# Performance work log

Measured on AMD Instinct MI355X. Metric: run time of the kernel, lower is better.

Reference implementation:

```python
import jax, jax.numpy as jnp
import numpy as np
from functools import partial

FACTOR = 5
N_HEADS = 16


def setup_inputs() -> dict:
    key = jax.random.key(0)
    ks = jax.random.split(key, 8)
    B, L, D = 4, 4096, 1024
    scale = 0.02
    return {
        "q": jax.random.normal(ks[0], (B, L, D), jnp.float32),
        "k": jax.random.normal(ks[1], (B, L, D), jnp.float32),
        "v": jax.random.normal(ks[2], (B, L, D), jnp.float32),
        "Wq": jax.random.normal(ks[3], (D, D), jnp.float32) * scale,
        "bq": jnp.zeros((D,), jnp.float32),
        "Wk": jax.random.normal(ks[4], (D, D), jnp.float32) * scale,
        "bk": jnp.zeros((D,), jnp.float32),
        "Wv": jax.random.normal(ks[5], (D, D), jnp.float32) * scale,
        "bv": jnp.zeros((D,), jnp.float32),
        "Wo": jax.random.normal(ks[6], (D, D), jnp.float32) * scale,
        "bo": jnp.zeros((D,), jnp.float32),
    }


def _time_delay_agg(values, corr):
    # values, corr: (B, H, L, C).  Faithful to the repo: the double mean
    # over dim=1 reduces head then LENGTH, leaving (B, C); top-k indices
    # therefore live in [0, C) and are reused as time delays.
    B, H, L, C = values.shape
    top_k = int(FACTOR * np.log(L + 1)) if L > 1 else 1
    top_k = max(1, min(top_k, L))
    mean_value = corr.mean(axis=1).mean(axis=1)          # (B, C)
    mean_across_batch = mean_value.mean(axis=0)          # (C,)
    actual_k = min(top_k, C)
    _, indices = jax.lax.top_k(mean_across_batch, actual_k)  # (k,)
    selected = mean_value[:, indices]                    # (B, k)
    weights = jax.nn.softmax(selected, axis=-1)          # (B, k)
    t = jnp.arange(L)

    def body(acc, inp):
        d, w = inp                                       # scalar delay, (B,) weight
        idx = (t + d) % L                                # circular shift == roll of doubled tensor
        acc = acc + values[:, :, idx, :] * w[:, None, None, None]
        return acc, None

    agg, _ = jax.lax.scan(body, jnp.zeros_like(values), (indices, weights.T))
    return agg


def reference(q, k, v, Wq, bq, Wk, bk, Wv, bv, Wo, bo):
    B, L, D = q.shape
    H = N_HEADS
    dk = D // H

    def proj(x, W, b):
        y = x @ W.T + b
        return y.reshape(B, L, H, dk).transpose(0, 2, 1, 3)  # (B,H,L,dk)

    Q = proj(q, Wq, bq).astype(jnp.float32)
    K = proj(k, Wk, bk).astype(jnp.float32)
    V = proj(v, Wv, bv).astype(jnp.float32)

    Qf = jnp.fft.rfft(Q, axis=2)
    Kf = jnp.fft.rfft(K, axis=2)
    R = jnp.fft.irfft(Qf * jnp.conj(Kf), n=L, axis=2)    # (B,H,L,dk) autocorrelation

    V_agg = _time_delay_agg(V, R)                        # (B,H,L,dk)
    V_agg = V_agg.transpose(0, 2, 1, 3).reshape(B, L, D)
    return V_agg @ Wo.T + bo
```

## Files before the change

kernel.cpp:

```cpp
#include <hip/hip_runtime.h>
#include <hip/hip_bf16.h>

#define Bn 4
#define Ln 4096
#define Dn 1024
#define Hn 16
#define KSEL 41
#define NT8 16

typedef __attribute__((ext_vector_type(8))) _Float16 f16x8;
typedef __attribute__((ext_vector_type(4))) float f32x4;

__device__ __forceinline__ unsigned short f2h(float f) {
    union { _Float16 h; unsigned short u; } c;
    c.h = (_Float16)f;
    return c.u;
}

__device__ __forceinline__ void gl2lds16(const unsigned short* g, unsigned short* l) {
    __builtin_amdgcn_global_load_lds(
        (const __attribute__((address_space(1))) unsigned int*)(uintptr_t)g,
        (__attribute__((address_space(3))) unsigned int*)(uintptr_t)l,
        16, 0, 0);
}
__device__ __forceinline__ void gl2lds16f(const float* g, float* l) {
    __builtin_amdgcn_global_load_lds(
        (const __attribute__((address_space(1))) unsigned int*)(uintptr_t)g,
        (__attribute__((address_space(3))) unsigned int*)(uintptr_t)l,
        16, 0, 0);
}

__global__ __launch_bounds__(256) void prework(const float* __restrict__ q,
                                               const float* __restrict__ k,
                                               const float* __restrict__ Wq_unused,
                                               const float* __restrict__ Wo,
                                               const float* __restrict__ Wv,
                                               const float* __restrict__ bv,
                                               const float* __restrict__ bo,
                                               float* __restrict__ part,
                                               unsigned short* __restrict__ Wcf,
                                               float* __restrict__ bc) {
    __shared__ __align__(16) unsigned short sAB[2][64 * 32];
    int bid = blockIdx.x;
    int tid = threadIdx.x;

    if (bid < 512) {
        int cx = bid & 63, tb = bid >> 6;
        int tensor = tb >> 2, b = tb & 3;
        const f32x4* src = (const f32x4*)((tensor ? k : q) + (size_t)b * Ln * Dn) + tid;
        int t0 = cx * 64;
        f32x4 a0 = (f32x4){0.f, 0.f, 0.f, 0.f};
        f32x4 a1 = (f32x4){0.f, 0.f, 0.f, 0.f};
        #pragma unroll 1
        for (int g = 0; g < 8; ++g) {
            const f32x4* p = src + (size_t)(t0 + g * 8) * 256;
            f32x4 v0 = __builtin_nontemporal_load(p + 0 * 256);
            f32x4 v1 = __builtin_nontemporal_load(p + 1 * 256);
            f32x4 v2 = __builtin_nontemporal_load(p + 2 * 256);
            f32x4 v3 = __builtin_nontemporal_load(p + 3 * 256);
            f32x4 v4 = __builtin_nontemporal_load(p + 4 * 256);
            f32x4 v5 = __builtin_nontemporal_load(p + 5 * 256);
            f32x4 v6 = __builtin_nontemporal_load(p + 6 * 256);
            f32x4 v7 = __builtin_nontemporal_load(p + 7 * 256);
            a0 += v0 + v2 + v4 + v6;
            a1 += v1 + v3 + v5 + v7;
        }
        f32x4 o = a0 + a1;
        ((f32x4*)part)[((size_t)tb * 64 + cx) * 256 + tid] = o;
    } else if (bid < 768) {
        unsigned short* sA = sAB[0];
        unsigned short* sB = sAB[1];
        int b2 = bid - 512;
        int n0 = (b2 >> 4) * 64, k0 = (b2 & 15) * 64;
        const int wv = tid >> 6, lane = tid & 63;
        const int wr = wv >> 1, wc = wv & 1;
        const int lrow = lane & 15, lk = (lane >> 4) * 8;
        const int ar0 = tid >> 3,  ac0 = (tid & 7) * 4;
        const int ar1 = (tid + 256) >> 3, ac1 = ((tid + 256) & 7) * 4;
        const int jr0 = tid >> 4,  kc0 = (tid & 15) * 4;
        const int jr1 = (tid + 256) >> 4, kc1 = ((tid + 256) & 15) * 4;
        f32x4 acc[2][2];
        #pragma unroll
        for (int i = 0; i < 2; ++i)
            #pragma unroll
            for (int j = 0; j < 2; ++j) acc[i][j] = (f32x4){0.f, 0.f, 0.f, 0.f};

        float4 avA, avB, bvA, bvB;
        auto LOADW = [&](int j0) {
            avA = *(const float4*)&Wo[(size_t)(n0 + ar0) * 1024 + j0 + ac0];
            avB = *(const float4*)&Wo[(size_t)(n0 + ar1) * 1024 + j0 + ac1];
            bvA = *(const float4*)&Wv[(size_t)(j0 + jr0) * 1024 + k0 + kc0];
            bvB = *(const float4*)&Wv[(size_t)(j0 + jr1) * 1024 + k0 + kc1];
        };
        LOADW(0);
        #pragma unroll 1
        for (int it = 0; it < 32; ++it) {
            ushort4 h;
            h.x = f2h(avA.x); h.y = f2h(avA.y); h.z = f2h(avA.z); h.w = f2h(avA.w);
            *(ushort4*)&sA[ar0 * 32 + ac0] = h;
            h.x = f2h(avB.x); h.y = f2h(avB.y); h.z = f2h(avB.z); h.w = f2h(avB.w);
            *(ushort4*)&sA[ar1 * 32 + ac1] = h;
            sB[(kc0 + 0) * 32 + jr0] = f2h(bvA.x);
            sB[(kc0 + 1) * 32 + jr0] = f2h(bvA.y);
            sB[(kc0 + 2) * 32 + jr0] = f2h(bvA.z);
            sB[(kc0 + 3) * 32 + jr0] = f2h(bvA.w);
            sB[(kc1 + 0) * 32 + jr1] = f2h(bvB.x);
            sB[(kc1 + 1) * 32 + jr1] = f2h(bvB.y);
            sB[(kc1 + 2) * 32 + jr1] = f2h(bvB.z);
            sB[(kc1 + 3) * 32 + jr1] = f2h(bvB.w);
            __syncthreads();
            if (it + 1 < 32) LOADW((it + 1) * 32);
            f16x8 af[2], bf[2];
            #pragma unroll
            for (int i = 0; i < 2; ++i)
                af[i] = *(const f16x8*)&sA[(wr * 32 + i * 16 + lrow) * 32 + lk];
            #pragma unroll
            for (int j = 0; j < 2; ++j)
                bf[j] = *(const f16x8*)&sB[(wc * 32 + j * 16 + lrow) * 32 + lk];
            #pragma unroll
            for (int i = 0; i < 2; ++i)
                #pragma unroll
                for (int j = 0; j < 2; ++j)
                    acc[i][j] = __builtin_amdgcn_mfma_f32_16x16x32_f16(af[i], bf[j], acc[i][j], 0, 0, 0);
            __syncthreads();
        }
        #pragma unroll
        for (int i = 0; i < 2; ++i) {
            int r0 = n0 + wr * 32 + i * 16 + (lane >> 4) * 4;
            #pragma unroll
            for (int j = 0; j < 2; ++j) {
                int c = k0 + wc * 32 + j * 16 + (lane & 15);
                #pragma unroll
                for (int r = 0; r < 4; ++r)
                    Wcf[(size_t)(r0 + r) * 1024 + c] = f2h(acc[i][j][r]);
            }
        }
    } else {
        float* s_bv = (float*)sAB;
        int b3 = bid - 768;
        for (int i = tid; i < 1024; i += 256) s_bv[i] = bv[i];
        __syncthreads();
        int wv2 = tid >> 6, lane = tid & 63;
        for (int rr = 0; rr < 4; ++rr) {
            int n = b3 * 16 + rr * 4 + wv2;
            float p = 0.f;
            for (int c = 0; c < 4; ++c) {
                float4 w4 = *(const float4*)(Wo + (size_t)n * 1024 + c * 256 + lane * 4);
                float4 s4 = *(const float4*)(s_bv + c * 256 + lane * 4);
                p += w4.x * s4.x + w4.y * s4.y + w4.z * s4.z + w4.w * s4.w;
            }
            for (int off = 1; off < 64; off <<= 1) p += __shfl_xor(p, off);
            if (lane == 0) bc[n] = p + bo[n];
        }
    }
}

__global__ void colsum_fin(const float* __restrict__ part, float* __restrict__ sums) {
    int tb = blockIdx.y; int d = blockIdx.x * 256 + threadIdx.x;
    float s = 0.f;
    for (int i = 0; i < 64; ++i) s += part[((size_t)tb * 64 + i) * 1024 + d];
    sums[(size_t)tb * 1024 + d] = s;
}

__global__ void proj_sums(const float* __restrict__ sums,
                          const float* __restrict__ Wq, const float* __restrict__ bq,
                          const float* __restrict__ Wk, const float* __restrict__ bk,
                          float* __restrict__ SQK) {
    int t = blockIdx.y;
    const float* W    = t ? Wk : Wq;
    const float* bias = t ? bk : bq;
    const float* sv   = sums + (size_t)t * 4 * 1024;
    __shared__ float s_sv[4 * 1024];
    for (int i = threadIdx.x; i < 4 * 1024; i += 256) s_sv[i] = sv[i];
    __syncthreads();
    int wave = threadIdx.x >> 6, lane = threadIdx.x & 63;
    for (int rr = 0; rr < 4; ++rr) {
        int j = blockIdx.x * 16 + rr * 4 + wave;
        float p[4] = {0.f, 0.f, 0.f, 0.f};
        for (int c = 0; c < 4; ++c) {
            float4 wv = *(const float4*)(W + (size_t)j * 1024 + c * 256 + lane * 4);
            #pragma unroll
            for (int b = 0; b < 4; ++b) {
                float4 s = *(const float4*)(s_sv + b * 1024 + c * 256 + lane * 4);
                p[b] += wv.x * s.x + wv.y * s.y + wv.z * s.z + wv.w * s.w;
            }
        }
        #pragma unroll
        for (int b = 0; b < 4; ++b)
            for (int off = 1; off < 64; off <<= 1) p[b] += __shfl_xor(p[b], off);
        if (lane == 0) {
            float bb = bias[j] * (float)Ln;
            #pragma unroll
            for (int b = 0; b < 4; ++b) SQK[((size_t)t * 4 + b) * 1024 + j] = p[b] + bb;
        }
    }
}

__global__ void stats_topk(const float* __restrict__ SQK, int* __restrict__ dly,
                           float* __restrict__ gp) {
    __shared__ float s_mv[4][64];
    __shared__ float mab[64];
    __shared__ float selv[4][KSEL];
    __shared__ int   s_dly[KSEL];
    int tid = threadIdx.x; int b = tid >> 6, c = tid & 63;
    const float* SQ = SQK; const float* SK = SQK + 4 * 1024;
    float s = 0.f;
    for (int h = 0; h < Hn; ++h)
        s += SQ[(size_t)b * 1024 + h * 64 + c] * SK[(size_t)b * 1024 + h * 64 + c];
    s_mv[b][c] = s * (1.0f / ((float)Hn * (float)Ln));
    __syncthreads();
    if (tid < 64) mab[c] = (s_mv[0][c] + s_mv[1][c] + s_mv[2][c] + s_mv[3][c]) * 0.25f;
    __syncthreads();
    if (tid < 64) {
        float my = mab[c];
        int rank = 0;
        for (int j = 0; j < 64; ++j) {
            float vj = mab[j];
            rank += (vj > my) || (vj == my && j < c);
        }
        if (rank < KSEL) {
            s_dly[rank] = c;
            dly[rank] = c;
            selv[0][rank] = s_mv[0][c]; selv[1][rank] = s_mv[1][c];
            selv[2][rank] = s_mv[2][c]; selv[3][rank] = s_mv[3][c];
        }
    }
    __syncthreads();
    if (tid < 256) gp[tid] = 0.f;
    __syncthreads();
    if (tid < 4) {
        float mx = -1e30f;
        for (int i = 0; i < KSEL; ++i) mx = fmaxf(mx, selv[tid][i]);
        float ss = 0.f;
        for (int i = 0; i < KSEL; ++i) ss += expf(selv[tid][i] - mx);
        float inv = 1.0f / ss;
        for (int i = 0; i < KSEL; ++i)
            gp[tid * 64 + s_dly[i]] = expf(selv[tid][i] - mx) * inv;
    }
}

#define FT 128
#define FC 64
#define FW 64
__global__ __launch_bounds__(256) void gather_fir(const float* __restrict__ v,
                                                  const float* __restrict__ gp,
                                                  unsigned short* __restrict__ Vf) {
    __shared__ float S[(FT + FW) * FC];
    int b = blockIdx.z, c0 = blockIdx.y * FC, t0 = blockIdx.x * FT;
    const float* Vb = v + (size_t)b * Ln * Dn;
    #pragma unroll
    for (int it = 0; it < 12; ++it) {
        int idx = it * 256 + threadIdx.x;
        int r = idx >> 4, cc = idx & 15;
        int gr = (t0 + r) & (Ln - 1);
        gl2lds16f(Vb + (size_t)gr * Dn + c0 + cc * 4, S + idx * 4);
    }
    __syncthreads();
    int c4 = threadIdx.x & 15, rg = threadIdx.x >> 4;
    const int base = rg * 8;
    float4 acc[8];
    #pragma unroll
    for (int i = 0; i < 8; ++i) acc[i] = make_float4(0.f, 0.f, 0.f, 0.f);
    #pragma unroll
    for (int tc = 0; tc < 2; ++tc) {
        float gc[32];
        #pragma unroll
        for (int j = 0; j < 8; ++j) {
            float4 gv = ((const float4*)(gp + b * 64 + tc * 32))[j];
            gc[j * 4 + 0] = gv.x; gc[j * 4 + 1] = gv.y;
            gc[j * 4 + 2] = gv.z; gc[j * 4 + 3] = gv.w;
        }
        #pragma unroll
        for (int w = 0; w < 39; ++w) {
            float4 x = *(const float4*)&S[(base + tc * 32 + w) * FC + c4 * 4];
            #pragma unroll
            for (int i = 0; i < 8; ++i) {
                int j = w - i;
                if (j >= 0 && j < 32) {
                    float wt = gc[j];
                    acc[i].x += wt * x.x; acc[i].y += wt * x.y;
                    acc[i].z += wt * x.z; acc[i].w += wt * x.w;
                }
            }
        }
    }
    #pragma unroll
    for (int i = 0; i < 8; ++i) {
        size_t idx = ((size_t)b * Ln + t0 + base + i) * Dn + c0 + c4 * 4;
        ushort4 o;
        o.x = f2h(acc[i].x); o.y = f2h(acc[i].y);
        o.z = f2h(acc[i].z); o.w = f2h(acc[i].w);
        *(ushort4*)&Vf[idx] = o;
    }
}

__device__ __forceinline__ void mm16q(const f16x8* a, const f16x8* b, f32x4 (&acc)[2][4]) {
    #pragma unroll
    for (int i = 0; i < 2; ++i)
        #pragma unroll
        for (int j = 0; j < 4; ++j)
            #pragma unroll
            for (int s = 0; s < 2; ++s)
                acc[i][j] = __builtin_amdgcn_mfma_f32_16x16x32_f16(a[i * 2 + s], b[j * 2 + s],
                                                                   acc[i][j], 0, 0, 0);
}

__global__ __launch_bounds__(512, 2) void gemm8p(const unsigned short* __restrict__ A,
                                                 const unsigned short* __restrict__ Bt,
                                                 float* __restrict__ C,
                                                 const float* __restrict__ bias) {
    __shared__ unsigned short lds[65536];
    int bid = blockIdx.x;
    int swz = (bid & 7) * 32 + (bid >> 3);
    int by = swz >> 2, bx = swz & 3;

    const int tid = threadIdx.x;
    const int wv = tid >> 6, lane = tid & 63;
    const int wr = wv >> 1, wc = wv & 1;
    const int srow = lane >> 3, sslot = lane & 7;

    f32x4 acc[4][2][4];
    #pragma unroll
    for (int q = 0; q < 4; ++q)
        #pragma unroll
        for (int i = 0; i < 2; ++i)
            #pragma unroll
            for (int j = 0; j < 4; ++j) acc[q][i][j] = (f32x4){0.f, 0.f, 0.f, 0.f};

    auto STAGE = [&](int t, int op, int mh) {
        unsigned short* hb = lds + ((((t & 1) * 2 + op) * 2 + mh) << 13);
        const unsigned short* G = op ? Bt : A;
        int base_row = (op ? bx : by) * 256 + mh * 128;
        #pragma unroll
        for (int i = 0; i < 2; ++i) {
            int rl = i * 64 + wv * 8 + srow;
            int cs = sslot ^ (rl & 7);
            gl2lds16(G + (size_t)(base_row + rl) * 1024 + t * 64 + cs * 8,
                     hb + i * 4096 + wv * 512);
        }
    };
    auto LDA = [&](int t, int h, f16x8* a) {
        const unsigned short* hb = lds + ((((t & 1) * 2 + 0) * 2 + h) << 13);
        #pragma unroll
        for (int i = 0; i < 2; ++i) {
            int rl = wr * 32 + i * 16 + (lane & 15);
            #pragma unroll
            for (int s = 0; s < 2; ++s) {
                int cs = s * 4 + (lane >> 4);
                a[i * 2 + s] = *(const f16x8*)(hb + rl * 64 + ((cs ^ (rl & 7)) << 3));
            }
        }
    };
    auto LDB = [&](int t, int h, f16x8* b) {
        const unsigned short* hb = lds + ((((t & 1) * 2 + 1) * 2 + h) << 13);
        #pragma unroll
        for (int j = 0; j < 4; ++j) {
            int rl = wc * 64 + j * 16 + (lane & 15);
            #pragma unroll
            for (int s = 0; s < 2; ++s) {
                int cs = s * 4 + (lane >> 4);
                b[j * 2 + s] = *(const f16x8*)(hb + rl * 64 + ((cs ^ (rl & 7)) << 3));
            }
        }
    };

    STAGE(0, 0, 0); STAGE(0, 1, 0); STAGE(0, 0, 1); STAGE(0, 1, 1);
    STAGE(1, 0, 0); STAGE(1, 1, 0); STAGE(1, 0, 1);
    asm volatile("s_waitcnt vmcnt(6)" ::: "memory");
    __builtin_amdgcn_s_barrier();

    f16x8 a0[4], a1[4], b[8];
    for (int t = 0; t < NT8; ++t) {
        const bool p1 = (t + 1 < NT8), p2 = (t + 2 < NT8);
        LDA(t, 0, a0); LDB(t, 0, b);
        if (p1) STAGE(t + 1, 1, 1);
        __builtin_amdgcn_s_barrier();
        asm volatile("s_waitcnt lgkmcnt(0)" ::: "memory");
        __builtin_amdgcn_sched_barrier(0);
        __builtin_amdgcn_s_setprio(1);
        mm16q(a0, b, acc[0]);
        __builtin_amdgcn_s_setprio(0);
        __builtin_amdgcn_s_barrier();
        LDA(t, 1, a1);
        if (p2) STAGE(t + 2, 0, 0);
        __builtin_amdgcn_s_barrier();
        asm volatile("s_waitcnt lgkmcnt(0)" ::: "memory");
        __builtin_amdgcn_sched_barrier(0);
        __builtin_amdgcn_s_setprio(1);
        mm16q(a1, b, acc[2]);
        __builtin_amdgcn_s_setprio(0);
        __builtin_amdgcn_s_barrier();
        LDB(t, 1, b);
        if (p2) STAGE(t + 2, 1, 0);
        __builtin_amdgcn_s_barrier();
        asm volatile("s_waitcnt lgkmcnt(0)" ::: "memory");
        __builtin_amdgcn_sched_barrier(0);
        __builtin_amdgcn_s_setprio(1);
        mm16q(a0, b, acc[1]);
        __builtin_amdgcn_s_setprio(0);
        __builtin_amdgcn_s_barrier();
        if (p2) STAGE(t + 2, 0, 1);
        if (p2) { asm volatile("s_waitcnt vmcnt(6)" ::: "memory"); }
        else    { asm volatile("s_waitcnt vmcnt(0)" ::: "memory"); }
        __builtin_amdgcn_s_barrier();
        __builtin_amdgcn_s_setprio(1);
        mm16q(a1, b, acc[3]);
        __builtin_amdgcn_s_setprio(0);
        __builtin_amdgcn_s_barrier();
    }

    const int lr = (lane >> 4) << 2, lc = lane & 15;
    #pragma unroll
    for (int q = 0; q < 4; ++q) {
        int rbase = by * 256 + (q >> 1) * 128 + wr * 32 + lr;
        int cbase = bx * 256 + (q & 1) * 128 + wc * 64 + lc;
        #pragma unroll
        for (int j = 0; j < 4; ++j) {
            int c = cbase + j * 16;
            float bb = bias[c];
            #pragma unroll
            for (int i = 0; i < 2; ++i)
                #pragma unroll
                for (int r = 0; r < 4; ++r)
                    C[(size_t)(rbase + i * 16 + r) * 1024 + c] = acc[q][i][j][r] + bb;
        }
    }
}

extern "C" void kernel_launch(void* const* d_in, const int* in_sizes, int n_in,
                              void* d_out, int out_size, void* d_ws, size_t ws_size,
                              hipStream_t stream) {
    const float* q  = (const float*)d_in[0];
    const float* k  = (const float*)d_in[1];
    const float* v  = (const float*)d_in[2];
    const float* Wq = (const float*)d_in[3];
    const float* bq = (const float*)d_in[4];
    const float* Wk = (const float*)d_in[5];
    const float* bk = (const float*)d_in[6];
    const float* Wv = (const float*)d_in[7];
    const float* bv = (const float*)d_in[8];
    const float* Wo = (const float*)d_in[9];
    const float* bo = (const float*)d_in[10];
    float* out = (float*)d_out;
    float* ws  = (float*)d_ws;

    unsigned short* Vf  = (unsigned short*)ws;
    unsigned short* Wcf = Vf + 16777216;
    float* part = (float*)(Wcf + 1048576);
    float* sums = part + 524288;
    float* SQK  = sums + 8192;
    float* gp   = SQK + 8192;
    float* bc   = gp + 256;
    int*   dly  = (int*)(bc + 1024);

    hipLaunchKernelGGL(prework, dim3(832), dim3(256), 0, stream,
                       q, k, Wq, Wo, Wv, bv, bo, part, Wcf, bc);

    hipLaunchKernelGGL(colsum_fin, dim3(4, 8), dim3(256), 0, stream, part, sums);
    hipLaunchKernelGGL(proj_sums, dim3(64, 2), dim3(256), 0, stream, sums, Wq, bq, Wk, bk, SQK);
    hipLaunchKernelGGL(stats_topk, dim3(1), dim3(256), 0, stream, SQK, dly, gp);

    hipLaunchKernelGGL(gather_fir, dim3(32, 16, 4), dim3(256), 0, stream, v, gp, Vf);

    hipLaunchKernelGGL(gemm8p, dim3(256), dim3(512), 0, stream, Vf, Wcf, out, bc);
}
```

Before: 135.7 us.

## Split column-sum reduction into many small blocks using direct global-to-LDS loads

The q/k column-sum stage now uses 4096 blocks of 8 rows each instead of 512 blocks of 64 rows. Each block pulls its rows into shared memory with global_load_lds and sums them there. The goal is more memory-level parallelism and better occupancy while streaming 128MB of q/k. In exchange, the partial-sum buffer grows eightfold, 16MB of extra writes and reads, and colsum_fin must now serially reduce 512 partials per column in only 32 blocks, which could become a new bottleneck. Block roles are reordered so the GEMM and bias blocks come first.

```diff
diff --git a/kernel.cpp b/kernel.cpp
--- a/kernel.cpp
+++ b/kernel.cpp
@@ -32,7 +32,6 @@
 
 __global__ __launch_bounds__(256) void prework(const float* __restrict__ q,
                                                const float* __restrict__ k,
-                                               const float* __restrict__ Wq_unused,
                                                const float* __restrict__ Wo,
                                                const float* __restrict__ Wv,
                                                const float* __restrict__ bv,
@@ -40,38 +39,30 @@
                                                float* __restrict__ part,
                                                unsigned short* __restrict__ Wcf,
                                                float* __restrict__ bc) {
-    __shared__ __align__(16) unsigned short sAB[2][64 * 32];
+    __shared__ __align__(16) float S[8 * 1024];
     int bid = blockIdx.x;
     int tid = threadIdx.x;
 
-    if (bid < 512) {
-        int cx = bid & 63, tb = bid >> 6;
+    if (bid >= 320) {
+        int cid = bid - 320;
+        int tb = cid >> 9, cx = cid & 511;
         int tensor = tb >> 2, b = tb & 3;
-        const f32x4* src = (const f32x4*)((tensor ? k : q) + (size_t)b * Ln * Dn) + tid;
-        int t0 = cx * 64;
-        f32x4 a0 = (f32x4){0.f, 0.f, 0.f, 0.f};
-        f32x4 a1 = (f32x4){0.f, 0.f, 0.f, 0.f};
-        #pragma unroll 1
-        for (int g = 0; g < 8; ++g) {
-            const f32x4* p = src + (size_t)(t0 + g * 8) * 256;
-            f32x4 v0 = __builtin_nontemporal_load(p + 0 * 256);
-            f32x4 v1 = __builtin_nontemporal_load(p + 1 * 256);
-            f32x4 v2 = __builtin_nontemporal_load(p + 2 * 256);
-            f32x4 v3 = __builtin_nontemporal_load(p + 3 * 256);
-            f32x4 v4 = __builtin_nontemporal_load(p + 4 * 256);
-            f32x4 v5 = __builtin_nontemporal_load(p + 5 * 256);
-            f32x4 v6 = __builtin_nontemporal_load(p + 6 * 256);
-            f32x4 v7 = __builtin_nontemporal_load(p + 7 * 256);
-            a0 += v0 + v2 + v4 + v6;
-            a1 += v1 + v3 + v5 + v7;
-        }
-        f32x4 o = a0 + a1;
-        ((f32x4*)part)[((size_t)tb * 64 + cx) * 256 + tid] = o;
-    } else if (bid < 768) {
-        unsigned short* sA = sAB[0];
-        unsigned short* sB = sAB[1];
-        int b2 = bid - 512;
-        int n0 = (b2 >> 4) * 64, k0 = (b2 & 15) * 64;
+        const float* src = (tensor ? k : q) + (size_t)b * Ln * Dn + (size_t)(cx * 8) * Dn;
+        float* ls = &S[tid * 4];
+        #pragma unroll
+        for (int i = 0; i < 8; ++i)
+            gl2lds16f(src + (size_t)i * Dn + tid * 4, ls + i * 1024);
+        asm volatile("s_waitcnt vmcnt(0)" ::: "memory");
+        __builtin_amdgcn_s_barrier();
+        f32x4 acc = (f32x4){0.f, 0.f, 0.f, 0.f};
+        #pragma unroll
+        for (int i = 0; i < 8; ++i)
+            acc += *(const f32x4*)&S[tid * 4 + i * 1024];
+        ((f32x4*)part)[((size_t)tb * 512 + cx) * 256 + tid] = acc;
+    } else if (bid < 256) {
+        unsigned short* sA = (unsigned short*)S;
+        unsigned short* sB = (unsigned short*)S + 64 * 32;
+        int n0 = (bid >> 4) * 64, k0 = (bid & 15) * 64;
         const int wv = tid >> 6, lane = tid & 63;
         const int wr = wv >> 1, wc = wv & 1;
         const int lrow = lane & 15, lk = (lane >> 4) * 8;
@@ -136,8 +127,8 @@
             }
         }
     } else {
-        float* s_bv = (float*)sAB;
-        int b3 = bid - 768;
+        float* s_bv = S;
+        int b3 = bid - 256;
         for (int i = tid; i < 1024; i += 256) s_bv[i] = bv[i];
         __syncthreads();
         int wv2 = tid >> 6, lane = tid & 63;
@@ -158,7 +149,7 @@
 __global__ void colsum_fin(const float* __restrict__ part, float* __restrict__ sums) {
     int tb = blockIdx.y; int d = blockIdx.x * 256 + threadIdx.x;
     float s = 0.f;
-    for (int i = 0; i < 64; ++i) s += part[((size_t)tb * 64 + i) * 1024 + d];
+    for (int i = 0; i < 512; ++i) s += part[((size_t)tb * 512 + i) * 1024 + d];
     sums[(size_t)tb * 1024 + d] = s;
 }
 
@@ -447,14 +438,14 @@
     unsigned short* Vf  = (unsigned short*)ws;
     unsigned short* Wcf = Vf + 16777216;
     float* part = (float*)(Wcf + 1048576);
-    float* sums = part + 524288;
+    float* sums = part + 4194304;
     float* SQK  = sums + 8192;
     float* gp   = SQK + 8192;
     float* bc   = gp + 256;
     int*   dly  = (int*)(bc + 1024);
 
-    hipLaunchKernelGGL(prework, dim3(832), dim3(256), 0, stream,
-                       q, k, Wq, Wo, Wv, bv, bo, part, Wcf, bc);
+    hipLaunchKernelGGL(prework, dim3(4416), dim3(256), 0, stream,
+                       q, k, Wo, Wv, bv, bo, part, Wcf, bc);
 
     hipLaunchKernelGGL(colsum_fin, dim3(4, 8), dim3(256), 0, stream, part, sums);
     hipLaunchKernelGGL(proj_sums, dim3(64, 2), dim3(256), 0, stream, sums, Wq, bq, Wk, bk, SQK);
```

Measured after the change: 157.0 us. 1.16x slower.

## Apply combined projection GEMM before delay aggregation and fuse with column sums

Applied to the files above, without the earlier changes.

Uses linearity to swap the order of the delay-weighted FIR aggregation and the output GEMM. V is multiplied by the combined Wo·Wv weight first, in a new simpler 128x128-tile GEMM that converts fp32 V to fp16 on the fly. The GEMM runs in the same launch as the q/k column-sum blocks, so it overlaps the top-k statistics path. The FIR gather then reads the fp16 GEMM output, adds the bias and writes fp32 output directly, removing the separate fp16 Vf pass and the heavily pipelined gemm8p. The trade-off is a less tuned GEMM (no double buffering, more syncs) and an extra rounding step before the aggregation.

```diff
diff --git a/kernel.cpp b/kernel.cpp
--- a/kernel.cpp
+++ b/kernel.cpp
@@ -6,9 +6,9 @@
 #define Dn 1024
 #define Hn 16
 #define KSEL 41
-#define NT8 16
 
 typedef __attribute__((ext_vector_type(8))) _Float16 f16x8;
+typedef __attribute__((ext_vector_type(4))) _Float16 f16x4;
 typedef __attribute__((ext_vector_type(4))) float f32x4;
 
 __device__ __forceinline__ unsigned short f2h(float f) {
@@ -23,55 +23,20 @@
         (__attribute__((address_space(3))) unsigned int*)(uintptr_t)l,
         16, 0, 0);
 }
-__device__ __forceinline__ void gl2lds16f(const float* g, float* l) {
-    __builtin_amdgcn_global_load_lds(
-        (const __attribute__((address_space(1))) unsigned int*)(uintptr_t)g,
-        (__attribute__((address_space(3))) unsigned int*)(uintptr_t)l,
-        16, 0, 0);
-}
-
-__global__ __launch_bounds__(256) void prework(const float* __restrict__ q,
-                                               const float* __restrict__ k,
-                                               const float* __restrict__ Wq_unused,
-                                               const float* __restrict__ Wo,
-                                               const float* __restrict__ Wv,
-                                               const float* __restrict__ bv,
-                                               const float* __restrict__ bo,
-                                               float* __restrict__ part,
-                                               unsigned short* __restrict__ Wcf,
-                                               float* __restrict__ bc) {
-    __shared__ __align__(16) unsigned short sAB[2][64 * 32];
+
+__global__ __launch_bounds__(256) void prepA(const float* __restrict__ Wo,
+                                             const float* __restrict__ Wv,
+                                             const float* __restrict__ bv,
+                                             const float* __restrict__ bo,
+                                             unsigned short* __restrict__ Wcf,
+                                             float* __restrict__ bc) {
+    __shared__ __align__(16) float S[2048];
     int bid = blockIdx.x;
     int tid = threadIdx.x;
-
-    if (bid < 512) {
-        int cx = bid & 63, tb = bid >> 6;
-        int tensor = tb >> 2, b = tb & 3;
-        const f32x4* src = (const f32x4*)((tensor ? k : q) + (size_t)b * Ln * Dn) + tid;
-        int t0 = cx * 64;
-        f32x4 a0 = (f32x4){0.f, 0.f, 0.f, 0.f};
-        f32x4 a1 = (f32x4){0.f, 0.f, 0.f, 0.f};
-        #pragma unroll 1
-        for (int g = 0; g < 8; ++g) {
-            const f32x4* p = src + (size_t)(t0 + g * 8) * 256;
-            f32x4 v0 = __builtin_nontemporal_load(p + 0 * 256);
-            f32x4 v1 = __builtin_nontemporal_load(p + 1 * 256);
-            f32x4 v2 = __builtin_nontemporal_load(p + 2 * 256);
-            f32x4 v3 = __builtin_nontemporal_load(p + 3 * 256);
-            f32x4 v4 = __builtin_nontemporal_load(p + 4 * 256);
-            f32x4 v5 = __builtin_nontemporal_load(p + 5 * 256);
-            f32x4 v6 = __builtin_nontemporal_load(p + 6 * 256);
-            f32x4 v7 = __builtin_nontemporal_load(p + 7 * 256);
-            a0 += v0 + v2 + v4 + v6;
-            a1 += v1 + v3 + v5 + v7;
-        }
-        f32x4 o = a0 + a1;
-        ((f32x4*)part)[((size_t)tb * 64 + cx) * 256 + tid] = o;
-    } else if (bid < 768) {
-        unsigned short* sA = sAB[0];
-        unsigned short* sB = sAB[1];
-        int b2 = bid - 512;
-        int n0 = (b2 >> 4) * 64, k0 = (b2 & 15) * 64;
+    if (bid < 256) {
+        unsigned short* sA = (unsigned short*)S;
+        unsigned short* sB = (unsigned short*)S + 64 * 32;
+        int n0 = (bid >> 4) * 64, k0 = (bid & 15) * 64;
         const int wv = tid >> 6, lane = tid & 63;
         const int wr = wv >> 1, wc = wv & 1;
         const int lrow = lane & 15, lk = (lane >> 4) * 8;
@@ -84,7 +49,6 @@
         for (int i = 0; i < 2; ++i)
             #pragma unroll
             for (int j = 0; j < 2; ++j) acc[i][j] = (f32x4){0.f, 0.f, 0.f, 0.f};
-
         float4 avA, avB, bvA, bvB;
         auto LOADW = [&](int j0) {
             avA = *(const float4*)&Wo[(size_t)(n0 + ar0) * 1024 + j0 + ac0];
@@ -136,8 +100,8 @@
             }
         }
     } else {
-        float* s_bv = (float*)sAB;
-        int b3 = bid - 768;
+        float* s_bv = S;
+        int b3 = bid - 256;
         for (int i = tid; i < 1024; i += 256) s_bv[i] = bv[i];
         __syncthreads();
         int wv2 = tid >> 6, lane = tid & 63;
@@ -152,6 +116,114 @@
             for (int off = 1; off < 64; off <<= 1) p += __shfl_xor(p, off);
             if (lane == 0) bc[n] = p + bo[n];
         }
+    }
+}
+
+__global__ __launch_bounds__(256) void mainwork(const float* __restrict__ v,
+                                                const float* __restrict__ q,
+                                                const float* __restrict__ k,
+                                                const unsigned short* __restrict__ Wcf,
+                                                unsigned short* __restrict__ Of,
+                                                float* __restrict__ part) {
+    __shared__ __align__(16) unsigned short sAB[8192];
+    int bid = blockIdx.x;
+    int tid = threadIdx.x;
+
+    if (bid < 1024) {
+        unsigned short* sA = sAB;
+        unsigned short* sB = sAB + 4096;
+        int swz = (bid & 7) * 128 + (bid >> 3);
+        int by = swz >> 3, bx = swz & 7;
+
+        const int wave = tid >> 6, lane = tid & 63;
+        const int lrow = lane & 15, lk = (lane >> 4) * 8;
+        const int wr = wave >> 1, wc = wave & 1;
+        const int arow = tid >> 3, acol = (tid & 7) * 4;
+        const int srow = lane >> 2, skq = (lane & 3) * 8;
+
+        f32x4 acc[4][4];
+        #pragma unroll
+        for (int i = 0; i < 4; ++i)
+            #pragma unroll
+            for (int j = 0; j < 4; ++j) acc[i][j] = (f32x4){0.f, 0.f, 0.f, 0.f};
+
+        const float* Av = v + (size_t)(by * 128) * 1024;
+        float4 p0, p1, p2, p3;
+        auto LOADA = [&](int k0) {
+            p0 = *(const float4*)&Av[(size_t)(0 * 32 + arow) * 1024 + k0 + acol];
+            p1 = *(const float4*)&Av[(size_t)(1 * 32 + arow) * 1024 + k0 + acol];
+            p2 = *(const float4*)&Av[(size_t)(2 * 32 + arow) * 1024 + k0 + acol];
+            p3 = *(const float4*)&Av[(size_t)(3 * 32 + arow) * 1024 + k0 + acol];
+        };
+        LOADA(0);
+        #pragma unroll 1
+        for (int it = 0; it < 32; ++it) {
+            int k0 = it * 32;
+            ushort4 h;
+            h.x = f2h(p0.x); h.y = f2h(p0.y); h.z = f2h(p0.z); h.w = f2h(p0.w);
+            *(ushort4*)&sA[(0 * 32 + arow) * 32 + acol] = h;
+            h.x = f2h(p1.x); h.y = f2h(p1.y); h.z = f2h(p1.z); h.w = f2h(p1.w);
+            *(ushort4*)&sA[(1 * 32 + arow) * 32 + acol] = h;
+            h.x = f2h(p2.x); h.y = f2h(p2.y); h.z = f2h(p2.z); h.w = f2h(p2.w);
+            *(ushort4*)&sA[(2 * 32 + arow) * 32 + acol] = h;
+            h.x = f2h(p3.x); h.y = f2h(p3.y); h.z = f2h(p3.z); h.w = f2h(p3.w);
+            *(ushort4*)&sA[(3 * 32 + arow) * 32 + acol] = h;
+            #pragma unroll
+            for (int j = 0; j < 2; ++j) {
+                int chunk = j * 4 + wave;
+                int row = chunk * 16 + srow;
+                gl2lds16(Wcf + (size_t)(bx * 128 + row) * 1024 + k0 + skq, sB + chunk * 512);
+            }
+            __syncthreads();
+            if (it + 1 < 32) LOADA(k0 + 32);
+            f16x8 bfrag[4];
+            #pragma unroll
+            for (int j = 0; j < 4; ++j)
+                bfrag[j] = *(const f16x8*)&sB[(wc * 64 + j * 16 + lrow) * 32 + lk];
+            #pragma unroll
+            for (int i = 0; i < 4; ++i) {
+                f16x8 afrag = *(const f16x8*)&sA[(wr * 64 + i * 16 + lrow) * 32 + lk];
+                #pragma unroll
+                for (int j = 0; j < 4; ++j)
+                    acc[i][j] = __builtin_amdgcn_mfma_f32_16x16x32_f16(afrag, bfrag[j], acc[i][j], 0, 0, 0);
+            }
+            __syncthreads();
+        }
+        #pragma unroll
+        for (int i = 0; i < 4; ++i) {
+            int r0 = by * 128 + wr * 64 + i * 16 + (lane >> 4) * 4;
+            #pragma unroll
+            for (int j = 0; j < 4; ++j) {
+                int c = bx * 128 + wc * 64 + j * 16 + (lane & 15);
+                #pragma unroll
+                for (int r = 0; r < 4; ++r)
+                    Of[(size_t)(r0 + r) * 1024 + c] = f2h(acc[i][j][r]);
+            }
+        }
+    } else {
+        int cid = bid - 1024;
+        int cx = cid & 63, tb = cid >> 6;
+        int tensor = tb >> 2, b = tb & 3;
+        const f32x4* src = (const f32x4*)((tensor ? k : q) + (size_t)b * Ln * Dn) + tid;
+        int t0 = cx * 64;
+        f32x4 a0 = (f32x4){0.f, 0.f, 0.f, 0.f};
+        f32x4 a1 = (f32x4){0.f, 0.f, 0.f, 0.f};
+        #pragma unroll 1
+        for (int g = 0; g < 8; ++g) {
+            const f32x4* p = src + (size_t)(t0 + g * 8) * 256;
+            f32x4 v0 = __builtin_nontemporal_load(p + 0 * 256);
+            f32x4 v1 = __builtin_nontemporal_load(p + 1 * 256);
+            f32x4 v2 = __builtin_nontemporal_load(p + 2 * 256);
+            f32x4 v3 = __builtin_nontemporal_load(p + 3 * 256);
+            f32x4 v4 = __builtin_nontemporal_load(p + 4 * 256);
+            f32x4 v5 = __builtin_nontemporal_load(p + 5 * 256);
+            f32x4 v6 = __builtin_nontemporal_load(p + 6 * 256);
+            f32x4 v7 = __builtin_nontemporal_load(p + 7 * 256);
+            a0 += v0 + v2 + v4 + v6;
+            a1 += v1 + v3 + v5 + v7;
+        }
+        f32x4 o = a0 + a1;
+        ((f32x4*)part)[((size_t)tb * 64 + cx) * 256 + tid] = o;
     }
 }
 
@@ -242,18 +314,19 @@
 #define FT 128
 #define FC 64
 #define FW 64
-__global__ __launch_bounds__(256) void gather_fir(const float* __restrict__ v,
-                                                  const float* __restrict__ gp,
-                                                  unsigned short* __restrict__ Vf) {
-    __shared__ float S[(FT + FW) * FC];
+__global__ __launch_bounds__(256) void gather_o(const unsigned short* __restrict__ Of,
+                                                const float* __restrict__ gp,
+                                                const float* __restrict__ bc,
+                                                float* __restrict__ out) {
+    __shared__ unsigned short S[(FT + FW) * FC];
     int b = blockIdx.z, c0 = blockIdx.y * FC, t0 = blockIdx.x * FT;
-    const float* Vb = v + (size_t)b * Ln * Dn;
+    const unsigned short* Ob = Of + (size_t)b * Ln * Dn;
     #pragma unroll
-    for (int it = 0; it < 12; ++it) {
+    for (int it = 0; it < 6; ++it) {
         int idx = it * 256 + threadIdx.x;
-        int r = idx >> 4, cc = idx & 15;
+        int r = idx >> 3, cc = idx & 7;
         int gr = (t0 + r) & (Ln - 1);
-        gl2lds16f(Vb + (size_t)gr * Dn + c0 + cc * 4, S + idx * 4);
+        gl2lds16(Ob + (size_t)gr * 1024 + c0 + cc * 8, S + idx * 8);
     }
     __syncthreads();
     int c4 = threadIdx.x & 15, rg = threadIdx.x >> 4;
@@ -272,158 +345,26 @@
         }
         #pragma unroll
         for (int w = 0; w < 39; ++w) {
-            float4 x = *(const float4*)&S[(base + tc * 32 + w) * FC + c4 * 4];
+            f16x4 hv = *(const f16x4*)&S[(base + tc * 32 + w) * FC + c4 * 4];
+            float x0 = (float)hv[0], x1 = (float)hv[1], x2 = (float)hv[2], x3 = (float)hv[3];
             #pragma unroll
             for (int i = 0; i < 8; ++i) {
                 int j = w - i;
                 if (j >= 0 && j < 32) {
                     float wt = gc[j];
-                    acc[i].x += wt * x.x; acc[i].y += wt * x.y;
-                    acc[i].z += wt * x.z; acc[i].w += wt * x.w;
+                    acc[i].x += wt * x0; acc[i].y += wt * x1;
+                    acc[i].z += wt * x2; acc[i].w += wt * x3;
                 }
             }
         }
     }
+    float4 bias = *(const float4*)&bc[c0 + c4 * 4];
     #pragma unroll
     for (int i = 0; i < 8; ++i) {
-        size_t idx = ((size_t)b * Ln + t0 + base + i) * Dn + c0 + c4 * 4;
-        ushort4 o;
-        o.x = f2h(acc[i].x); o.y = f2h(acc[i].y);
-        o.z = f2h(acc[i].z); o.w = f2h(acc[i].w);
-        *(ushort4*)&Vf[idx] = o;
-    }
-}
-
-__device__ __forceinline__ void mm16q(const f16x8* a, const f16x8* b, f32x4 (&acc)[2][4]) {
-    #pragma unroll
-    for (int i = 0; i < 2; ++i)
-        #pragma unroll
-        for (int j = 0; j < 4; ++j)
-            #pragma unroll
-            for (int s = 0; s < 2; ++s)
-                acc[i][j] = __builtin_amdgcn_mfma_f32_16x16x32_f16(a[i * 2 + s], b[j * 2 + s],
-                                                                   acc[i][j], 0, 0, 0);
-}
-
-__global__ __launch_bounds__(512, 2) void gemm8p(const unsigned short* __restrict__ A,
-                                                 const unsigned short* __restrict__ Bt,
-                                                 float* __restrict__ C,
-                                                 const float* __restrict__ bias) {
-    __shared__ unsigned short lds[65536];
-    int bid = blockIdx.x;
-    int swz = (bid & 7) * 32 + (bid >> 3);
-    int by = swz >> 2, bx = swz & 3;
-
-    const int tid = threadIdx.x;
-    const int wv = tid >> 6, lane = tid & 63;
-    const int wr = wv >> 1, wc = wv & 1;
-    const int srow = lane >> 3, sslot = lane & 7;
-
-    f32x4 acc[4][2][4];
-    #pragma unroll
-    for (int q = 0; q < 4; ++q)
-        #pragma unroll
-        for (int i = 0; i < 2; ++i)
-            #pragma unroll
-            for (int j = 0; j < 4; ++j) acc[q][i][j] = (f32x4){0.f, 0.f, 0.f, 0.f};
-
-    auto STAGE = [&](int t, int op, int mh) {
-        unsigned short* hb = lds + ((((t & 1) * 2 + op) * 2 + mh) << 13);
-        const unsigned short* G = op ? Bt : A;
-        int base_row = (op ? bx : by) * 256 + mh * 128;
-        #pragma unroll
-        for (int i = 0; i < 2; ++i) {
-            int rl = i * 64 + wv * 8 + srow;
-            int cs = sslot ^ (rl & 7);
-            gl2lds16(G + (size_t)(base_row + rl) * 1024 + t * 64 + cs * 8,
-                     hb + i * 4096 + wv * 512);
-        }
-    };
-    auto LDA = [&](int t, int h, f16x8* a) {
-        const unsigned short* hb = lds + ((((t & 1) * 2 + 0) * 2 + h) << 13);
-        #pragma unroll
-        for (int i = 0; i < 2; ++i) {
-            int rl = wr * 32 + i * 16 + (lane & 15);
-            #pragma unroll
-            for (int s = 0; s < 2; ++s) {
-                int cs = s * 4 + (lane >> 4);
-                a[i * 2 + s] = *(const f16x8*)(hb + rl * 64 + ((cs ^ (rl & 7)) << 3));
-            }
-        }
-    };
-    auto LDB = [&](int t, int h, f16x8* b) {
-        const unsigned short* hb = lds + ((((t & 1) * 2 + 1) * 2 + h) << 13);
-        #pragma unroll
-        for (int j = 0; j < 4; ++j) {
-            int rl = wc * 64 + j * 16 + (lane & 15);
-            #pragma unroll
-            for (int s = 0; s < 2; ++s) {
-                int cs = s * 4 + (lane >> 4);
-                b[j * 2 + s] = *(const f16x8*)(hb + rl * 64 + ((cs ^ (rl & 7)) << 3));
-            }
-        }
-    };
-
-    STAGE(0, 0, 0); STAGE(0, 1, 0); STAGE(0, 0, 1); STAGE(0, 1, 1);
-    STAGE(1, 0, 0); STAGE(1, 1, 0); STAGE(1, 0, 1);
-    asm volatile("s_waitcnt vmcnt(6)" ::: "memory");
-    __builtin_amdgcn_s_barrier();
-
-    f16x8 a0[4], a1[4], b[8];
-    for (int t = 0; t < NT8; ++t) {
-        const bool p1 = (t + 1 < NT8), p2 = (t + 2 < NT8);
-        LDA(t, 0, a0); LDB(t, 0, b);
-        if (p1) STAGE(t + 1, 1, 1);
-        __builtin_amdgcn_s_barrier();
-        asm volatile("s_waitcnt lgkmcnt(0)" ::: "memory");
-        __builtin_amdgcn_sched_barrier(0);
-        __builtin_amdgcn_s_setprio(1);
-        mm16q(a0, b, acc[0]);
-        __builtin_amdgcn_s_setprio(0);
-        __builtin_amdgcn_s_barrier();
-        LDA(t, 1, a1);
-        if (p2) STAGE(t + 2, 0, 0);
-        __builtin_amdgcn_s_barrier();
-        asm volatile("s_waitcnt lgkmcnt(0)" ::: "memory");
-        __builtin_amdgcn_sched_barrier(0);
-        __builtin_amdgcn_s_setprio(1);
-        mm16q(a1, b, acc[2]);
-        __builtin_amdgcn_s_setprio(0);
-        __builtin_amdgcn_s_barrier();
-        LDB(t, 1, b);
-        if (p2) STAGE(t + 2, 1, 0);
-        __builtin_amdgcn_s_barrier();
-        asm volatile("s_waitcnt lgkmcnt(0)" ::: "memory");
-        __builtin_amdgcn_sched_barrier(0);
-        __builtin_amdgcn_s_setprio(1);
-        mm16q(a0, b, acc[1]);
-        __builtin_amdgcn_s_setprio(0);
-        __builtin_amdgcn_s_barrier();
-        if (p2) STAGE(t + 2, 0, 1);
-        if (p2) { asm volatile("s_waitcnt vmcnt(6)" ::: "memory"); }
-        else    { asm volatile("s_waitcnt vmcnt(0)" ::: "memory"); }
-        __builtin_amdgcn_s_barrier();
-        __builtin_amdgcn_s_setprio(1);
-        mm16q(a1, b, acc[3]);
-        __builtin_amdgcn_s_setprio(0);
-        __builtin_amdgcn_s_barrier();
-    }
-
-    const int lr = (lane >> 4) << 2, lc = lane & 15;
-    #pragma unroll
-    for (int q = 0; q < 4; ++q) {
-        int rbase = by * 256 + (q >> 1) * 128 + wr * 32 + lr;
-        int cbase = bx * 256 + (q & 1) * 128 + wc * 64 + lc;
-        #pragma unroll
-        for (int j = 0; j < 4; ++j) {
-            int c = cbase + j * 16;
-            float bb = bias[c];
-            #pragma unroll
-            for (int i = 0; i < 2; ++i)
-                #pragma unroll
-                for (int r = 0; r < 4; ++r)
-                    C[(size_t)(rbase + i * 16 + r) * 1024 + c] = acc[q][i][j][r] + bb;
-        }
+        float4 o;
+        o.x = acc[i].x + bias.x; o.y = acc[i].y + bias.y;
+        o.z = acc[i].z + bias.z; o.w = acc[i].w + bias.w;
+        *(float4*)&out[((size_t)b * Ln + t0 + base + i) * Dn + c0 + c4 * 4] = o;
     }
 }
 
@@ -444,8 +385,8 @@
     float* out = (float*)d_out;
     float* ws  = (float*)d_ws;
 
-    unsigned short* Vf  = (unsigned short*)ws;
-    unsigned short* Wcf = Vf + 16777216;
+    unsigned short* Of  = (unsigned short*)ws;
+    unsigned short* Wcf = Of + 16777216;
     float* part = (float*)(Wcf + 1048576);
     float* sums = part + 524288;
     float* SQK  = sums + 8192;
@@ -453,14 +394,13 @@
     float* bc   = gp + 256;
     int*   dly  = (int*)(bc + 1024);
 
-    hipLaunchKernelGGL(prework, dim3(832), dim3(256), 0, stream,
-                       q, k, Wq, Wo, Wv, bv, bo, part, Wcf, bc);
+    hipLaunchKernelGGL(prepA, dim3(320), dim3(256), 0, stream, Wo, Wv, bv, bo, Wcf, bc);
+
+    hipLaunchKernelGGL(mainwork, dim3(1536), dim3(256), 0, stream, v, q, k, Wcf, Of, part);
 
     hipLaunchKernelGGL(colsum_fin, dim3(4, 8), dim3(256), 0, stream, part, sums);
     hipLaunchKernelGGL(proj_sums, dim3(64, 2), dim3(256), 0, stream, sums, Wq, bq, Wk, bk, SQK);
     hipLaunchKernelGGL(stats_topk, dim3(1), dim3(256), 0, stream, SQK, dly, gp);
 
-    hipLaunchKernelGGL(gather_fir, dim3(32, 16, 4), dim3(256), 0, stream, v, gp, Vf);
-
-    hipLaunchKernelGGL(gemm8p, dim3(256), dim3(512), 0, stream, Vf, Wcf, out, bc);
-}
+    hipLaunchKernelGGL(gather_o, dim3(32, 16, 4), dim3(256), 0, stream, Of, gp, bc, out);
+}
```

Result: slower. 158.8 us (+17.0%).
